# Kernel tuning notes

Hardware: AMD Instinct MI355X
Metric: run time of the kernel (lower is better)

## Reference

```python
import jax, jax.numpy as jnp
import numpy as np

B, TQ, TI, TT = 8, 256, 256, 256
H, NH, F, E = 1024, 16, 4096, 8
HD = H // NH
EPS = 1e-5


def _ln(x, g, b):
    m = x.mean(-1, keepdims=True)
    v = ((x - m) ** 2).mean(-1, keepdims=True)
    return (x - m) / jnp.sqrt(v + EPS) * g + b


def _mha(q, k, v, in_w, in_b, out_w, out_b):
    # torch nn.MultiheadAttention: packed in_proj [3H,H], out_proj [H,H]
    wq, wk, wv = jnp.split(in_w, 3, axis=0)
    bq, bk, bv = jnp.split(in_b, 3, axis=0)
    Bq, Tq, _ = q.shape
    Tk = k.shape[1]
    qh = (q @ wq.T + bq).reshape(Bq, Tq, NH, HD)
    kh = (k @ wk.T + bk).reshape(Bq, Tk, NH, HD)
    vh = (v @ wv.T + bv).reshape(Bq, Tk, NH, HD)
    scores = jnp.einsum('bqhd,bkhd->bhqk', qh, kh) / jnp.sqrt(jnp.float32(HD))
    attn = jax.nn.softmax(scores, axis=-1)
    out = jnp.einsum('bhqk,bkhd->bqhd', attn, vh).reshape(Bq, Tq, H)
    return out @ out_w.T + out_b


def _moe(x, w1, b1, w2, b2, probs):
    # dense all-expert FFN: GELU(x W1 + b1) W2 + b2, mixed by router probs
    h = jax.nn.gelu(jnp.einsum('bth,ehf->btef', x, w1) + b1, approximate=False)
    o = jnp.einsum('btef,efh->bteh', h, w2) + b2
    return (o * probs[..., None]).sum(axis=-2)


def setup_inputs() -> dict:
    key = jax.random.key(0)
    ks = jax.random.split(key, 24)
    s = 0.02
    d = {}
    d['query_tokens'] = jax.random.normal(ks[0], (B, TQ, H), jnp.float32)
    d['image_tokens'] = jax.random.normal(ks[1], (B, TI, H), jnp.float32)
    d['text_context'] = jax.random.normal(ks[2], (B, TT, H), jnp.float32)
    d['sa_in_w'] = jax.random.normal(ks[3], (3 * H, H), jnp.float32) * s
    d['sa_in_b'] = jnp.zeros((3 * H,), jnp.float32)
    d['sa_out_w'] = jax.random.normal(ks[4], (H, H), jnp.float32) * s
    d['sa_out_b'] = jnp.zeros((H,), jnp.float32)
    d['ca_in_w'] = jax.random.normal(ks[5], (3 * H, H), jnp.float32) * s
    d['ca_in_b'] = jnp.zeros((3 * H,), jnp.float32)
    d['ca_out_w'] = jax.random.normal(ks[6], (H, H), jnp.float32) * s
    d['ca_out_b'] = jnp.zeros((H,), jnp.float32)
    d['img_gate_w'] = jax.random.normal(ks[7], (E, 2 * H), jnp.float32) * s
    d['img_gate_b'] = jnp.zeros((E,), jnp.float32)
    d['txt_gate_w'] = jax.random.normal(ks[8], (E, 2 * H), jnp.float32) * s
    d['txt_gate_b'] = jnp.zeros((E,), jnp.float32)
    d['lnq_g'] = jnp.ones((H,), jnp.float32)
    d['lnq_b'] = jnp.zeros((H,), jnp.float32)
    d['lnc_g'] = jnp.ones((H,), jnp.float32)
    d['lnc_b'] = jnp.zeros((H,), jnp.float32)
    d['lnf_g'] = jnp.ones((H,), jnp.float32)
    d['lnf_b'] = jnp.zeros((H,), jnp.float32)
    d['ew1'] = jax.random.normal(ks[9], (E, H, F), jnp.float32) * s
    d['eb1'] = jnp.zeros((E, F), jnp.float32)
    d['ew2'] = jax.random.normal(ks[10], (E, F, H), jnp.float32) * s
    d['eb2'] = jnp.zeros((E, H), jnp.float32)
    return d


def reference(query_tokens, image_tokens, text_context,
              sa_in_w, sa_in_b, sa_out_w, sa_out_b,
              ca_in_w, ca_in_b, ca_out_w, ca_out_b,
              img_gate_w, img_gate_b, txt_gate_w, txt_gate_b,
              lnq_g, lnq_b, lnc_g, lnc_b, lnf_g, lnf_b,
              ew1, eb1, ew2, eb2):
    # self-attention on query stream (dropout is identity in eval)
    q_norm = _ln(query_tokens, lnq_g, lnq_b)
    query_tokens = query_tokens + _mha(q_norm, q_norm, q_norm, sa_in_w, sa_in_b, sa_out_w, sa_out_b)
    # cross-attention query -> image tokens
    cross_norm = _ln(query_tokens, lnc_g, lnc_b)
    query_tokens = query_tokens + _mha(cross_norm, image_tokens, image_tokens, ca_in_w, ca_in_b, ca_out_w, ca_out_b)
    # gating contexts
    image_ctx = image_tokens.mean(axis=1, keepdims=True)   # [B,1,H]
    text_ctx = text_context.mean(axis=1, keepdims=True)    # [B,1,H]
    img_gate_in = jnp.concatenate([image_tokens, jnp.broadcast_to(text_ctx, image_tokens.shape)], axis=-1)
    txt_gate_in = jnp.concatenate([query_tokens, jnp.broadcast_to(image_ctx, query_tokens.shape)], axis=-1)
    temp = jnp.maximum(jnp.float32(1.0), 0.001)  # router temperature buffer = 1.0
    image_probs = jax.nn.softmax((img_gate_in @ img_gate_w.T + img_gate_b) / temp, axis=-1)
    text_probs = jax.nn.softmax((txt_gate_in @ txt_gate_w.T + txt_gate_b) / temp, axis=-1)
    # dense MoE (ep_group is None -> all experts evaluated, mixed by full softmax)
    q_ffn = _ln(query_tokens, lnf_g, lnf_b)
    query_tokens = query_tokens + _moe(q_ffn, ew1, eb1, ew2, eb2, text_probs)
    image_tokens = image_tokens + _moe(image_tokens, ew1, eb1, ew2, eb2, image_probs)
    return query_tokens, image_tokens
```

## Files before the change

kernel.cpp:

```cpp
#include <hip/hip_runtime.h>
#include <math.h>

typedef unsigned short u16;
typedef __bf16 bf16x8 __attribute__((ext_vector_type(8)));
typedef float  f32x4  __attribute__((ext_vector_type(4)));
typedef unsigned short u16x8 __attribute__((ext_vector_type(8)));
typedef unsigned short u16x4 __attribute__((ext_vector_type(4)));

union B8 { u16x8 u; bf16x8 b; };

__device__ __forceinline__ u16 f2bf(float x) {
  unsigned int u = __float_as_uint(x);
  unsigned int r = (u + 0x7fffu + ((u >> 16) & 1u)) >> 16;
  return (u16)r;
}
__device__ __forceinline__ float bf2f(u16 h) {
  return __uint_as_float(((unsigned int)h) << 16);
}

__device__ __forceinline__ void gload16(const void* g, void* l) {
  __builtin_amdgcn_global_load_lds(
      (const __attribute__((address_space(1))) unsigned int*)g,
      (__attribute__((address_space(3))) unsigned int*)l, 16, 0, 0);
}

__device__ __forceinline__ void wait_tiles(int left) {
  if (left >= 2)      asm volatile("s_waitcnt vmcnt(8)" ::: "memory");
  else if (left == 1) asm volatile("s_waitcnt vmcnt(4)" ::: "memory");
  else                asm volatile("s_waitcnt vmcnt(0)" ::: "memory");
}

__global__ __launch_bounds__(256) void cast_kernel(const float* __restrict__ in,
                                                   u16* __restrict__ out, int n4) {
  int i = blockIdx.x * 256 + threadIdx.x;
  if (i >= n4) return;
  f32x4 v = *(const f32x4*)(in + (size_t)i * 4);
  u16x4 o;
  o[0] = f2bf(v[0]); o[1] = f2bf(v[1]); o[2] = f2bf(v[2]); o[3] = f2bf(v[3]);
  *(u16x4*)(out + (size_t)i * 4) = o;
}

__global__ void transpose_cast_kernel(const float* __restrict__ in, u16* __restrict__ out,
                                      int R, int C) {
  __shared__ float tile[32][33];
  int z = blockIdx.z;
  int r0 = blockIdx.y * 32, c0 = blockIdx.x * 32;
  const float* ip = in + (size_t)z * R * C;
  u16* op = out + (size_t)z * R * C;
  int tx = threadIdx.x, ty = threadIdx.y;
  #pragma unroll
  for (int i = 0; i < 32; i += 8)
    tile[ty + i][tx] = ip[(size_t)(r0 + ty + i) * C + c0 + tx];
  __syncthreads();
  #pragma unroll
  for (int i = 0; i < 32; i += 8)
    op[(size_t)(c0 + ty + i) * R + r0 + tx] = f2bf(tile[tx][ty + i]);
}

__global__ __launch_bounds__(256) void ln_kernel(const float* __restrict__ in,
                                                 const float* __restrict__ g,
                                                 const float* __restrict__ bt,
                                                 u16* __restrict__ out) {
  __shared__ float red[4];
  int row = blockIdx.x;
  int t = threadIdx.x;
  int lane = t & 63, wid = t >> 6;
  f32x4 x = *(const f32x4*)(in + (size_t)row * 1024 + t * 4);
  float s = x[0] + x[1] + x[2] + x[3];
  #pragma unroll
  for (int o = 32; o > 0; o >>= 1) s += __shfl_down(s, o, 64);
  if (lane == 0) red[wid] = s;
  __syncthreads();
  float mean = (red[0] + red[1] + red[2] + red[3]) * (1.0f / 1024.0f);
  __syncthreads();
  float d0 = x[0] - mean, d1 = x[1] - mean, d2 = x[2] - mean, d3 = x[3] - mean;
  float s2 = d0 * d0 + d1 * d1 + d2 * d2 + d3 * d3;
  #pragma unroll
  for (int o = 32; o > 0; o >>= 1) s2 += __shfl_down(s2, o, 64);
  if (lane == 0) red[wid] = s2;
  __syncthreads();
  float var = (red[0] + red[1] + red[2] + red[3]) * (1.0f / 1024.0f);
  float rstd = rsqrtf(var + 1e-5f);
  f32x4 gg = *(const f32x4*)(g + t * 4);
  f32x4 bb = *(const f32x4*)(bt + t * 4);
  u16x4 o;
  o[0] = f2bf(d0 * rstd * gg[0] + bb[0]);
  o[1] = f2bf(d1 * rstd * gg[1] + bb[1]);
  o[2] = f2bf(d2 * rstd * gg[2] + bb[2]);
  o[3] = f2bf(d3 * rstd * gg[3] + bb[3]);
  *(u16x4*)(out + (size_t)row * 1024 + t * 4) = o;
}

#define SRC_COL(t) ((((t) & 3) ^ (((t) >> 3) & 1) ^ ((((t) >> 4) & 1) << 1)) * 8)

template <int MODE>
__global__ __launch_bounds__(256, 2) void gemm_bt(const u16* __restrict__ A,
                                                  const u16* __restrict__ B,
                                                  const float* __restrict__ bias,
                                                  const float* __restrict__ extra,
                                                  void* __restrict__ out,
                                                  int M, int N, int K, int expert, int kChunk) {
  __shared__ u16 sm[32768];
  const int tid = threadIdx.x;
  const int lane = tid & 63;
  const int wid = tid >> 6;
  const int wr = wid >> 1, wc = wid & 1;
  const int l15 = lane & 15;
  const int kg = lane >> 4;
  const int kgr8 = (kg ^ ((lane >> 1) & 1) ^ (((lane >> 2) & 1) << 1)) * 8;

  const int nwg = gridDim.x * gridDim.y;
  const int bid = blockIdx.y * gridDim.x + blockIdx.x;
  const int swz = (bid & 7) * (nwg >> 3) + (bid >> 3);
  const int m0 = (swz / gridDim.x) * 128;
  const int n0 = (swz % gridDim.x) * 128;
  const int kOff = blockIdx.z * kChunk;

  f32x4 acc[4][4];
  #pragma unroll
  for (int i = 0; i < 4; i++)
    #pragma unroll
    for (int j = 0; j < 4; j++) acc[i][j] = f32x4{0.f, 0.f, 0.f, 0.f};

  const int sc = SRC_COL(tid);
  const u16* ga = A + (size_t)(m0 + (tid >> 2)) * K + sc + kOff;
  const u16* gb = B + (size_t)(n0 + (tid >> 2)) * K + sc + kOff;
  const size_t rowskip = (size_t)64 * K;

#define STG(b, kt)                                                  \
  do {                                                              \
    u16* d = sm + (b) * 8192 + wid * 512;                           \
    gload16(ga + (kt), d);                                          \
    gload16(ga + rowskip + (kt), d + 2048);                         \
    gload16(gb + (kt), d + 4096);                                   \
    gload16(gb + rowskip + (kt), d + 6144);                         \
  } while (0)

  const int NT = kChunk >> 5;
  STG(0, 0); STG(1, 32); STG(2, 64);
  for (int t = 0; t < NT; ++t) {
    wait_tiles(NT - 1 - t);
    __builtin_amdgcn_s_barrier();
    if (t + 3 < NT) STG((t + 3) & 3, (t + 3) * 32);
    __builtin_amdgcn_sched_barrier(0);
    __builtin_amdgcn_s_setprio(1);
    const u16* base = sm + (t & 3) * 8192;
    B8 af[4], bfr[4];
    #pragma unroll
    for (int i = 0; i < 4; i++) {
      af[i].u  = *(const u16x8*)(base + (wr * 64 + l15 + i * 16) * 32 + kgr8);
      bfr[i].u = *(const u16x8*)(base + 4096 + (wc * 64 + l15 + i * 16) * 32 + kgr8);
    }
    #pragma unroll
    for (int i = 0; i < 4; i++)
      #pragma unroll
      for (int j = 0; j < 4; j++)
        acc[i][j] = __builtin_amdgcn_mfma_f32_16x16x32_bf16(af[i].b, bfr[j].b, acc[i][j], 0, 0, 0);
    __builtin_amdgcn_s_setprio(0);
  }
#undef STG

  const bool z0 = (blockIdx.z == 0);
  const int orow0 = m0 + wr * 64 + (lane >> 4) * 4;
  const int ocol0 = n0 + wc * 64 + l15;

  if constexpr (MODE == 0) {
    __builtin_amdgcn_s_barrier();
    u16* rp = sm + wid * 1152;
    const int mrow0 = m0 + wr * 64;
    const int cbase = n0 + wc * 64;
    #pragma unroll
    for (int i = 0; i < 4; i++) {
      #pragma unroll
      for (int j = 0; j < 4; j++) {
        const float bb = bias[cbase + j * 16 + l15];
        #pragma unroll
        for (int p = 0; p < 4; p++)
          rp[((lane >> 4) * 4 + p) * 72 + j * 16 + l15] = f2bf(acc[i][j][p] + bb);
      }
      asm volatile("s_waitcnt lgkmcnt(0)" ::: "memory");
      #pragma unroll
      for (int rr = 0; rr < 4; rr++) {
        const int r16 = rr * 4 + (lane >> 4);
        u16x4 v4 = *(const u16x4*)&rp[r16 * 72 + l15 * 4];
        *(u16x4*)((u16*)out + (size_t)(mrow0 + i * 16 + r16) * N + cbase + l15 * 4) = v4;
      }
      asm volatile("s_waitcnt lgkmcnt(0)" ::: "memory");
    }
  } else {
    #pragma unroll
    for (int i = 0; i < 4; i++) {
      float pr_[4];
      if constexpr (MODE == 3) {
        #pragma unroll
        for (int p = 0; p < 4; p++)
          pr_[p] = extra[(size_t)(orow0 + i * 16 + p) * 8 + expert];
      }
      #pragma unroll
      for (int j = 0; j < 4; j++) {
        const int gcol = ocol0 + j * 16;
        const float bb = bias[gcol];
        #pragma unroll
        for (int p = 0; p < 4; p++) {
          const int grow = orow0 + i * 16 + p;
          const size_t off = (size_t)grow * N + gcol;
          float v = acc[i][j][p];
          if constexpr (MODE == 1) {
            atomicAdd(&((float*)out)[off], v + (z0 ? bb + extra[off] : 0.f));
          } else {
            atomicAdd(&((float*)out)[off], pr_[p] * (v + (z0 ? bb : 0.f)));
          }
        }
      }
    }
  }
}

__global__ __launch_bounds__(512, 2) void gemm256(const u16* __restrict__ A, int lda,
                                                  const u16* __restrict__ B, int ldb,
                                                  const float* __restrict__ bias,
                                                  void* __restrict__ out,
                                                  int N, int kChunk) {
  __shared__ u16 sm[65536];
  const int tid = threadIdx.x;
  const int lane = tid & 63;
  const int wid = tid >> 6;
  const int wr = wid >> 2;
  const int wc = wid & 3;
  const int l15 = lane & 15;
  const int kg = lane >> 4;
  const int kgr8 = (kg ^ ((lane >> 1) & 1) ^ (((lane >> 2) & 1) << 1)) * 8;

  const int nwg = gridDim.x * gridDim.y;
  const int bid = blockIdx.y * gridDim.x + blockIdx.x;
  const int swz = (bid & 7) * (nwg >> 3) + (bid >> 3);
  const int m0 = (swz / gridDim.x) * 256;
  const int n0 = (swz % gridDim.x) * 256;

  f32x4 acc[8][4];
  #pragma unroll
  for (int i = 0; i < 8; i++)
    #pragma unroll
    for (int j = 0; j < 4; j++) acc[i][j] = f32x4{0.f, 0.f, 0.f, 0.f};

  const int sc = SRC_COL(tid);
  const u16* ga = A + (size_t)(m0 + (tid >> 2)) * lda + sc;
  const u16* gb = B + (size_t)(n0 + (tid >> 2)) * ldb + sc;
  const size_t a128 = (size_t)128 * lda;
  const size_t b128 = (size_t)128 * ldb;

#define STG256(b, kt)                                               \
  do {                                                              \
    u16* d = sm + (b) * 16384 + wid * 512;                          \
    gload16(ga + (kt), d);                                          \
    gload16(ga + (kt) + a128, d + 4096);                            \
    gload16(gb + (kt), d + 8192);                                   \
    gload16(gb + (kt) + b128, d + 12288);                           \
  } while (0)

  const int NT = kChunk >> 5;
  STG256(0, 0); STG256(1, 32); STG256(2, 64);
  for (int t = 0; t < NT; ++t) {
    wait_tiles(NT - 1 - t);
    __builtin_amdgcn_s_barrier();
    if (t + 3 < NT) STG256((t + 3) & 3, (t + 3) * 32);
    __builtin_amdgcn_sched_barrier(0);
    __builtin_amdgcn_s_setprio(1);
    const u16* base = sm + (t & 3) * 16384;
    B8 af[8], bfr[4];
    #pragma unroll
    for (int j = 0; j < 4; j++)
      bfr[j].u = *(const u16x8*)(base + 8192 + (wc * 64 + l15 + j * 16) * 32 + kgr8);
    #pragma unroll
    for (int i = 0; i < 8; i++)
      af[i].u = *(const u16x8*)(base + (wr * 128 + l15 + i * 16) * 32 + kgr8);
    #pragma unroll
    for (int i = 0; i < 8; i++)
      #pragma unroll
      for (int j = 0; j < 4; j++)
        acc[i][j] = __builtin_amdgcn_mfma_f32_16x16x32_bf16(af[i].b, bfr[j].b, acc[i][j], 0, 0, 0);
    __builtin_amdgcn_s_setprio(0);
  }
#undef STG256

  __builtin_amdgcn_s_barrier();
  u16* rp = sm + wid * 1152;
  const int mrow0 = m0 + wr * 128;
  const int cbase = n0 + wc * 64;
  #pragma unroll
  for (int i = 0; i < 8; i++) {
    #pragma unroll
    for (int j = 0; j < 4; j++) {
      const float bb = bias[cbase + j * 16 + l15];
      #pragma unroll
      for (int p = 0; p < 4; p++) {
        float vb = acc[i][j][p] + bb;
        float ge = 0.5f * vb * (1.0f + erff(vb * 0.70710678118654752f));
        rp[((lane >> 4) * 4 + p) * 72 + j * 16 + l15] = f2bf(ge);
      }
    }
    asm volatile("s_waitcnt lgkmcnt(0)" ::: "memory");
    #pragma unroll
    for (int rr = 0; rr < 4; rr++) {
      const int r16 = rr * 4 + (lane >> 4);
      u16x4 v4 = *(const u16x4*)&rp[r16 * 72 + l15 * 4];
      *(u16x4*)((u16*)out + (size_t)(mrow0 + i * 16 + r16) * N + cbase + l15 * 4) = v4;
    }
    asm volatile("s_waitcnt lgkmcnt(0)" ::: "memory");
  }
}

__global__ __launch_bounds__(256) void attn_mfma(const u16* __restrict__ qb, int qs,
                                                 const u16* __restrict__ kb_, int ks,
                                                 const u16* __restrict__ vb, int vs,
                                                 u16* __restrict__ outp) {
  __shared__ u16 Ks[64][72];
  __shared__ u16 Vt[64][72];
  __shared__ u16 Pl[4][64][72];
  const int t = threadIdx.x;
  const int lane = t & 63;
  const int w = t >> 6;
  const int b = blockIdx.x >> 4;
  const int h = blockIdx.x & 15;
  const int lr = lane & 15;
  const int kg = lane >> 4;
  const size_t qrow0 = (size_t)b * 256 + w * 64;

  B8 qf[4][2];
  #pragma unroll
  for (int i = 0; i < 4; i++)
    #pragma unroll
    for (int kk = 0; kk < 2; kk++)
      qf[i][kk].u = *(const u16x8*)(qb + (qrow0 + i * 16 + lr) * qs + h * 64 + kk * 32 + kg * 8);

  f32x4 ao[4][4];
  float m_[4][4], l_[4][4];
  #pragma unroll
  for (int i = 0; i < 4; i++)
    #pragma unroll
    for (int n = 0; n < 4; n++) ao[i][n] = f32x4{0.f, 0.f, 0.f, 0.f};
  #pragma unroll
  for (int i = 0; i < 4; i++)
    #pragma unroll
    for (int p = 0; p < 4; p++) { m_[i][p] = -1e30f; l_[i][p] = 0.f; }

  for (int jt = 0; jt < 4; ++jt) {
    __syncthreads();
    {
      int r = t >> 2, c = (t & 3) * 16;
      const u16* src = kb_ + ((size_t)b * 256 + jt * 64 + r) * ks + h * 64 + c;
      *(u16x8*)&Ks[r][c] = *(const u16x8*)src;
      *(u16x8*)&Ks[r][c + 8] = *(const u16x8*)(src + 8);
      int jj = t & 63;
      const u16* vsrc = vb + ((size_t)b * 256 + jt * 64 + jj) * vs + h * 64 + w * 16;
      u16x8 v0 = *(const u16x8*)vsrc;
      u16x8 v1 = *(const u16x8*)(vsrc + 8);
      #pragma unroll
      for (int d = 0; d < 8; d++) Vt[w * 16 + d][jj] = v0[d];
      #pragma unroll
      for (int d = 0; d < 8; d++) Vt[w * 16 + 8 + d][jj] = v1[d];
    }
    __syncthreads();

    B8 kf[2][4];
    #pragma unroll
    for (int kk = 0; kk < 2; kk++)
      #pragma unroll
      for (int n = 0; n < 4; n++)
        kf[kk][n].u = *(const u16x8*)&Ks[n * 16 + lr][kk * 32 + kg * 8];

    #pragma unroll
    for (int i = 0; i < 4; i++) {
      f32x4 s[4];
      #pragma unroll
      for (int n = 0; n < 4; n++) s[n] = f32x4{0.f, 0.f, 0.f, 0.f};
      #pragma unroll
      for (int kk = 0; kk < 2; kk++)
        #pragma unroll
        for (int n = 0; n < 4; n++)
          s[n] = __builtin_amdgcn_mfma_f32_16x16x32_bf16(qf[i][kk].b, kf[kk][n].b, s[n], 0, 0, 0);
      #pragma unroll
      for (int p = 0; p < 4; p++) {
        float pm = fmaxf(fmaxf(s[0][p], s[1][p]), fmaxf(s[2][p], s[3][p])) * 0.125f;
        #pragma unroll
        for (int mk = 1; mk < 16; mk <<= 1) pm = fmaxf(pm, __shfl_xor(pm, mk, 16));
        float mn = fmaxf(m_[i][p], pm);
        float scl = __expf(m_[i][p] - mn);
        m_[i][p] = mn;
        float rs = 0.f;
        #pragma unroll
        for (int n = 0; n < 4; n++) {
          float e = __expf(s[n][p] * 0.125f - mn);
          Pl[w][i * 16 + kg * 4 + p][n * 16 + lr] = f2bf(e);
          rs += e;
        }
        #pragma unroll
        for (int mk = 1; mk < 16; mk <<= 1) rs += __shfl_xor(rs, mk, 16);
        l_[i][p] = l_[i][p] * scl + rs;
        #pragma unroll
        for (int n2 = 0; n2 < 4; n2++) ao[i][n2][p] *= scl;
      }
    }

    B8 vf[2][4];
    #pragma unroll
    for (int kk = 0; kk < 2; kk++)
      #pragma unroll
      for (int n2 = 0; n2 < 4; n2++)
        vf[kk][n2].u = *(const u16x8*)&Vt[n2 * 16 + lr][kk * 32 + kg * 8];
    #pragma unroll
    for (int i = 0; i < 4; i++) {
      #pragma unroll
      for (int kk = 0; kk < 2; kk++) {
        B8 pa;
        pa.u = *(const u16x8*)&Pl[w][i * 16 + lr][kk * 32 + kg * 8];
        #pragma unroll
        for (int n2 = 0; n2 < 4; n2++)
          ao[i][n2] = __builtin_amdgcn_mfma_f32_16x16x32_bf16(pa.b, vf[kk][n2].b, ao[i][n2], 0, 0, 0);
      }
    }
  }

  #pragma unroll
  for (int i = 0; i < 4; i++) {
    #pragma unroll
    for (int p = 0; p < 4; p++) {
      const float inv = 1.0f / l_[i][p];
      const size_t row = qrow0 + i * 16 + kg * 4 + p;
      #pragma unroll
      for (int n2 = 0; n2 < 4; n2++)
        outp[row * 1024 + h * 64 + n2 * 16 + lr] = f2bf(ao[i][n2][p] * inv);
    }
  }
}

__global__ __launch_bounds__(256) void mean2_kernel(const float* __restrict__ in,
                                                    float* __restrict__ out) {
  __shared__ float part[128];
  const int blk = blockIdx.x;
  const int b = blk >> 3, ch = blk & 7;
  const int t = threadIdx.x;
  const int col = ch * 128 + (t & 127);
  const int half = t >> 7;
  const float* p = in + (size_t)b * 262144 + (size_t)half * 131072 + col;
  float s = 0.f;
  for (int r = 0; r < 128; r++) s += p[(size_t)r * 1024];
  if (half) part[t & 127] = s;
  __syncthreads();
  if (!half) out[b * 1024 + col] = (s + part[t & 127]) * (1.0f / 256.0f);
}

__global__ __launch_bounds__(256) void gate_kernel(const float* __restrict__ x,
                                                   const float* __restrict__ ctx,
                                                   const float* __restrict__ gw,
                                                   const float* __restrict__ gb,
                                                   float* __restrict__ probs, int rowoff) {
  __shared__ float lg[8];
  const int tok = blockIdx.x;
  const int b = tok >> 8;
  const int t = threadIdx.x;
  const int e = t >> 5, sl = t & 31;
  const float* xr = x + (size_t)tok * 1024;
  const float* cr = ctx + (size_t)b * 1024;
  const float* wrow = gw + (size_t)e * 2048;
  float s = 0.f;
  for (int c = sl; c < 1024; c += 32) s += xr[c] * wrow[c] + cr[c] * wrow[1024 + c];
  #pragma unroll
  for (int o = 16; o > 0; o >>= 1) s += __shfl_down(s, o, 32);
  if (sl == 0) lg[e] = s + gb[e];
  __syncthreads();
  if (t == 0) {
    float mx = lg[0];
    #pragma unroll
    for (int i = 1; i < 8; i++) mx = fmaxf(mx, lg[i]);
    float ex[8], sum = 0.f;
    #pragma unroll
    for (int i = 0; i < 8; i++) { ex[i] = expf(lg[i] - mx); sum += ex[i]; }
    float inv = 1.0f / sum;
    #pragma unroll
    for (int i = 0; i < 8; i++) probs[(size_t)(rowoff + tok) * 8 + i] = ex[i] * inv;
  }
}

__global__ __launch_bounds__(256) void final_add_kernel(const float* __restrict__ q3,
                                                        const float* __restrict__ img,
                                                        const float* __restrict__ moe,
                                                        float* __restrict__ out) {
  size_t i = (size_t)blockIdx.x * 256 + threadIdx.x;
  f32x4 m4 = *(const f32x4*)(moe + i * 4);
  f32x4 a4 = (i < 524288) ? *(const f32x4*)(q3 + i * 4)
                          : *(const f32x4*)(img + (i - 524288) * 4);
  f32x4 r;
  r[0] = a4[0] + m4[0]; r[1] = a4[1] + m4[1]; r[2] = a4[2] + m4[2]; r[3] = a4[3] + m4[3];
  *(f32x4*)(out + i * 4) = r;
}

extern "C" void kernel_launch(void* const* d_in, const int* in_sizes, int n_in,
                              void* d_out, int out_size, void* d_ws, size_t ws_size,
                              hipStream_t stream) {
  const float* query_in = (const float*)d_in[0];
  const float* image_in = (const float*)d_in[1];
  const float* text_in  = (const float*)d_in[2];
  const float* sa_in_w  = (const float*)d_in[3];
  const float* sa_in_b  = (const float*)d_in[4];
  const float* sa_out_w = (const float*)d_in[5];
  const float* sa_out_b = (const float*)d_in[6];
  const float* ca_in_w  = (const float*)d_in[7];
  const float* ca_in_b  = (const float*)d_in[8];
  const float* ca_out_w = (const float*)d_in[9];
  const float* ca_out_b = (const float*)d_in[10];
  const float* img_gate_w = (const float*)d_in[11];
  const float* img_gate_b = (const float*)d_in[12];
  const float* txt_gate_w = (const float*)d_in[13];
  const float* txt_gate_b = (const float*)d_in[14];
  const float* lnq_g = (const float*)d_in[15];
  const float* lnq_b = (const float*)d_in[16];
  const float* lnc_g = (const float*)d_in[17];
  const float* lnc_b = (const float*)d_in[18];
  const float* lnf_g = (const float*)d_in[19];
  const float* lnf_b = (const float*)d_in[20];
  const float* ew1 = (const float*)d_in[21];
  const float* eb1 = (const float*)d_in[22];
  const float* ew2 = (const float*)d_in[23];
  const float* eb2 = (const float*)d_in[24];

  char* base = (char*)d_ws;
  size_t off = 0;
  auto alloc = [&](size_t bytes) -> char* {
    char* p = base + off;
    off += (bytes + 255) & ~(size_t)255;
    return p;
  };

  u16* wsa_in  = (u16*)alloc((size_t)3072 * 1024 * 2);
  u16* wsa_out = (u16*)alloc((size_t)1024 * 1024 * 2);
  u16* wca_in  = (u16*)alloc((size_t)3072 * 1024 * 2);
  u16* wca_out = (u16*)alloc((size_t)1024 * 1024 * 2);
  u16* w1T = (u16*)alloc((size_t)8 * 4096 * 1024 * 2);
  u16* w2T = (u16*)alloc((size_t)8 * 4096 * 1024 * 2);
  char* big = alloc((size_t)50331648);
  float* q3 = (float*)alloc((size_t)2048 * 1024 * 4);
  u16* xmoe = (u16*)alloc((size_t)4096 * 1024 * 2);
  float* probs = (float*)alloc((size_t)4096 * 8 * 4);
  float* ctx = (float*)alloc((size_t)2 * 8192 * 4);

  u16* h1      = (u16*)big;
  float* moeac = (float*)(big + 33554432);
  u16* qn      = (u16*)big;
  u16* qkv     = (u16*)(big + 4194304);
  u16* attn_o  = (u16*)(big + 16777216);
  float* q2    = (float*)(big + 20971520);
  u16* cnorm   = (u16*)(big + 29360128);
  u16* qca     = (u16*)(big + 33554432);
  u16* kvca    = (u16*)(big + 37748736);
  u16* img_bf  = xmoe + (size_t)2048 * 1024;

  cast_kernel<<<3072, 256, 0, stream>>>(sa_in_w, wsa_in, 786432);
  cast_kernel<<<1024, 256, 0, stream>>>(sa_out_w, wsa_out, 262144);
  cast_kernel<<<3072, 256, 0, stream>>>(ca_in_w, wca_in, 786432);
  cast_kernel<<<1024, 256, 0, stream>>>(ca_out_w, wca_out, 262144);
  transpose_cast_kernel<<<dim3(128, 32, 8), dim3(32, 8), 0, stream>>>(ew1, w1T, 1024, 4096);
  transpose_cast_kernel<<<dim3(32, 128, 8), dim3(32, 8), 0, stream>>>(ew2, w2T, 4096, 1024);
  cast_kernel<<<2048, 256, 0, stream>>>(image_in, img_bf, 524288);

  ln_kernel<<<2048, 256, 0, stream>>>(query_in, lnq_g, lnq_b, qn);
  gemm_bt<0><<<dim3(24, 16), 256, 0, stream>>>(qn, wsa_in, sa_in_b, nullptr, qkv, 2048, 3072, 1024, 0, 1024);
  attn_mfma<<<128, 256, 0, stream>>>(qkv, 3072, qkv + 1024, 3072, qkv + 2048, 3072, attn_o);
  hipMemsetAsync(q2, 0, (size_t)2048 * 1024 * 4, stream);
  gemm_bt<1><<<dim3(8, 16, 2), 256, 0, stream>>>(attn_o, wsa_out, sa_out_b, query_in, q2, 2048, 1024, 1024, 0, 512);

  ln_kernel<<<2048, 256, 0, stream>>>(q2, lnc_g, lnc_b, cnorm);
  gemm_bt<0><<<dim3(8, 16), 256, 0, stream>>>(cnorm, wca_in, ca_in_b, nullptr, qca, 2048, 1024, 1024, 0, 1024);
  gemm_bt<0><<<dim3(16, 16), 256, 0, stream>>>(img_bf, wca_in + (size_t)1024 * 1024,
                                               ca_in_b + 1024, nullptr, kvca, 2048, 2048, 1024, 0, 1024);
  attn_mfma<<<128, 256, 0, stream>>>(qca, 1024, kvca, 2048, kvca + 1024, 2048, attn_o);
  hipMemsetAsync(q3, 0, (size_t)2048 * 1024 * 4, stream);
  gemm_bt<1><<<dim3(8, 16, 2), 256, 0, stream>>>(attn_o, wca_out, ca_out_b, q2, q3, 2048, 1024, 1024, 0, 512);

  mean2_kernel<<<64, 256, 0, stream>>>(image_in, ctx);
  mean2_kernel<<<64, 256, 0, stream>>>(text_in, ctx + 8192);
  gate_kernel<<<2048, 256, 0, stream>>>(q3, ctx, txt_gate_w, txt_gate_b, probs, 0);
  gate_kernel<<<2048, 256, 0, stream>>>(image_in, ctx + 8192, img_gate_w, img_gate_b, probs, 2048);

  ln_kernel<<<2048, 256, 0, stream>>>(q3, lnf_g, lnf_b, xmoe);
  hipMemsetAsync(moeac, 0, (size_t)4096 * 1024 * 4, stream);
  for (int e = 0; e < 8; ++e) {
    gemm256<<<dim3(16, 16), 512, 0, stream>>>(xmoe, 1024, w1T + (size_t)e * 4194304, 1024,
                                              eb1 + (size_t)e * 4096, h1, 4096, 1024);
    gemm_bt<3><<<dim3(8, 32), 256, 0, stream>>>(h1, w2T + (size_t)e * 4194304,
                                                eb2 + (size_t)e * 1024, probs, moeac,
                                                4096, 1024, 4096, e, 4096);
  }

  final_add_kernel<<<4096, 256, 0, stream>>>(q3, image_in, moeac, (float*)d_out);
}
```

Measured before the change: 1.253 ms.

## Run MoE down-projection on split-K 256x256 GEMM with interleaved staged loads

The expert W2 GEMM moves from the 128x128 gemm_bt kernel to the 256x256 gemm256 kernel with 4-way split-K and atomic, probability-weighted accumulation. The gemm256 main loop is restructured: A and B tile prefetches are issued at separate points, the MFMA work is split into two halves with LDS fragment loads between them, and explicit vmcnt waits with barriers replace the wait_tiles helper. The LDS swizzle pattern is also simplified. This aims to raise MFMA utilisation and operand reuse for the large GEMMs, at the cost of more atomics and extra barriers per iteration.

```diff
diff --git a/kernel.cpp b/kernel.cpp
--- a/kernel.cpp
+++ b/kernel.cpp
@@ -91,7 +91,7 @@
   *(u16x4*)(out + (size_t)row * 1024 + t * 4) = o;
 }
 
-#define SRC_COL(t) ((((t) & 3) ^ (((t) >> 3) & 1) ^ ((((t) >> 4) & 1) << 1)) * 8)
+#define SRC_COL(t) ((((t) & 3) ^ (((t) >> 3) & 3)) * 8)
 
 template <int MODE>
 __global__ __launch_bounds__(256, 2) void gemm_bt(const u16* __restrict__ A,
@@ -107,7 +107,7 @@
   const int wr = wid >> 1, wc = wid & 1;
   const int l15 = lane & 15;
   const int kg = lane >> 4;
-  const int kgr8 = (kg ^ ((lane >> 1) & 1) ^ (((lane >> 2) & 1) << 1)) * 8;
+  const int kgr8 = (kg ^ ((lane >> 1) & 3)) * 8;
 
   const int nwg = gridDim.x * gridDim.y;
   const int bid = blockIdx.y * gridDim.x + blockIdx.x;
@@ -190,12 +190,6 @@
   } else {
     #pragma unroll
     for (int i = 0; i < 4; i++) {
-      float pr_[4];
-      if constexpr (MODE == 3) {
-        #pragma unroll
-        for (int p = 0; p < 4; p++)
-          pr_[p] = extra[(size_t)(orow0 + i * 16 + p) * 8 + expert];
-      }
       #pragma unroll
       for (int j = 0; j < 4; j++) {
         const int gcol = ocol0 + j * 16;
@@ -204,23 +198,20 @@
         for (int p = 0; p < 4; p++) {
           const int grow = orow0 + i * 16 + p;
           const size_t off = (size_t)grow * N + gcol;
-          float v = acc[i][j][p];
-          if constexpr (MODE == 1) {
-            atomicAdd(&((float*)out)[off], v + (z0 ? bb + extra[off] : 0.f));
-          } else {
-            atomicAdd(&((float*)out)[off], pr_[p] * (v + (z0 ? bb : 0.f)));
-          }
+          atomicAdd(&((float*)out)[off], acc[i][j][p] + (z0 ? bb + extra[off] : 0.f));
         }
       }
     }
   }
 }
 
+template <int MODE>
 __global__ __launch_bounds__(512, 2) void gemm256(const u16* __restrict__ A, int lda,
                                                   const u16* __restrict__ B, int ldb,
                                                   const float* __restrict__ bias,
+                                                  const float* __restrict__ extra,
                                                   void* __restrict__ out,
-                                                  int N, int kChunk) {
+                                                  int N, int kChunk, int expert) {
   __shared__ u16 sm[65536];
   const int tid = threadIdx.x;
   const int lane = tid & 63;
@@ -229,13 +220,14 @@
   const int wc = wid & 3;
   const int l15 = lane & 15;
   const int kg = lane >> 4;
-  const int kgr8 = (kg ^ ((lane >> 1) & 1) ^ (((lane >> 2) & 1) << 1)) * 8;
+  const int kgr8 = (kg ^ ((lane >> 1) & 3)) * 8;
 
   const int nwg = gridDim.x * gridDim.y;
   const int bid = blockIdx.y * gridDim.x + blockIdx.x;
   const int swz = (bid & 7) * (nwg >> 3) + (bid >> 3);
   const int m0 = (swz / gridDim.x) * 256;
   const int n0 = (swz % gridDim.x) * 256;
+  const int kOff = blockIdx.z * kChunk;
 
   f32x4 acc[8][4];
   #pragma unroll
@@ -244,69 +236,119 @@
     for (int j = 0; j < 4; j++) acc[i][j] = f32x4{0.f, 0.f, 0.f, 0.f};
 
   const int sc = SRC_COL(tid);
-  const u16* ga = A + (size_t)(m0 + (tid >> 2)) * lda + sc;
-  const u16* gb = B + (size_t)(n0 + (tid >> 2)) * ldb + sc;
+  const u16* ga = A + (size_t)(m0 + (tid >> 2)) * lda + sc + kOff;
+  const u16* gb = B + (size_t)(n0 + (tid >> 2)) * ldb + sc + kOff;
   const size_t a128 = (size_t)128 * lda;
   const size_t b128 = (size_t)128 * ldb;
 
-#define STG256(b, kt)                                               \
-  do {                                                              \
-    u16* d = sm + (b) * 16384 + wid * 512;                          \
-    gload16(ga + (kt), d);                                          \
-    gload16(ga + (kt) + a128, d + 4096);                            \
-    gload16(gb + (kt), d + 8192);                                   \
-    gload16(gb + (kt) + b128, d + 12288);                           \
-  } while (0)
-
   const int NT = kChunk >> 5;
-  STG256(0, 0); STG256(1, 32); STG256(2, 64);
+  #pragma unroll
+  for (int p = 0; p < 3; ++p) {
+    u16* dA = sm + p * 16384 + wid * 512;
+    u16* dB = dA + 8192;
+    const size_t kc = (size_t)p * 32;
+    gload16(ga + kc, dA); gload16(ga + kc + a128, dA + 4096);
+    gload16(gb + kc, dB); gload16(gb + kc + b128, dB + 4096);
+  }
+  asm volatile("s_waitcnt vmcnt(8)" ::: "memory");
+  __builtin_amdgcn_s_barrier();
+
   for (int t = 0; t < NT; ++t) {
-    wait_tiles(NT - 1 - t);
+    const u16* base = sm + (t & 3) * 16384;
+    const int pf = t + 3;
+    const size_t kc = (size_t)pf * 32;
+    if (pf < NT) {
+      u16* dA = sm + (pf & 3) * 16384 + wid * 512;
+      gload16(ga + kc, dA); gload16(ga + kc + a128, dA + 4096);
+    }
+    B8 bf[4], af[4];
+    #pragma unroll
+    for (int j = 0; j < 4; j++)
+      bf[j].u = *(const u16x8*)(base + 8192 + (wc * 64 + j * 16 + l15) * 32 + kgr8);
+    #pragma unroll
+    for (int i = 0; i < 4; i++)
+      af[i].u = *(const u16x8*)(base + (wr * 128 + i * 16 + l15) * 32 + kgr8);
     __builtin_amdgcn_s_barrier();
-    if (t + 3 < NT) STG256((t + 3) & 3, (t + 3) * 32);
+    asm volatile("s_waitcnt lgkmcnt(0)" ::: "memory");
     __builtin_amdgcn_sched_barrier(0);
     __builtin_amdgcn_s_setprio(1);
-    const u16* base = sm + (t & 3) * 16384;
-    B8 af[8], bfr[4];
-    #pragma unroll
-    for (int j = 0; j < 4; j++)
-      bfr[j].u = *(const u16x8*)(base + 8192 + (wc * 64 + l15 + j * 16) * 32 + kgr8);
-    #pragma unroll
-    for (int i = 0; i < 8; i++)
-      af[i].u = *(const u16x8*)(base + (wr * 128 + l15 + i * 16) * 32 + kgr8);
-    #pragma unroll
-    for (int i = 0; i < 8; i++)
+    #pragma unroll
+    for (int i = 0; i < 4; i++)
       #pragma unroll
       for (int j = 0; j < 4; j++)
-        acc[i][j] = __builtin_amdgcn_mfma_f32_16x16x32_bf16(af[i].b, bfr[j].b, acc[i][j], 0, 0, 0);
+        acc[i][j] = __builtin_amdgcn_mfma_f32_16x16x32_bf16(af[i].b, bf[j].b, acc[i][j], 0, 0, 0);
     __builtin_amdgcn_s_setprio(0);
-  }
-#undef STG256
-
-  __builtin_amdgcn_s_barrier();
-  u16* rp = sm + wid * 1152;
-  const int mrow0 = m0 + wr * 128;
-  const int cbase = n0 + wc * 64;
-  #pragma unroll
-  for (int i = 0; i < 8; i++) {
-    #pragma unroll
-    for (int j = 0; j < 4; j++) {
-      const float bb = bias[cbase + j * 16 + l15];
-      #pragma unroll
-      for (int p = 0; p < 4; p++) {
-        float vb = acc[i][j][p] + bb;
-        float ge = 0.5f * vb * (1.0f + erff(vb * 0.70710678118654752f));
-        rp[((lane >> 4) * 4 + p) * 72 + j * 16 + l15] = f2bf(ge);
-      }
-    }
+    if (pf < NT) {
+      u16* dB = sm + (pf & 3) * 16384 + 8192 + wid * 512;
+      gload16(gb + kc, dB); gload16(gb + kc + b128, dB + 4096);
+    }
+    B8 af2[4];
+    #pragma unroll
+    for (int i = 0; i < 4; i++)
+      af2[i].u = *(const u16x8*)(base + (wr * 128 + (i + 4) * 16 + l15) * 32 + kgr8);
+    __builtin_amdgcn_s_barrier();
     asm volatile("s_waitcnt lgkmcnt(0)" ::: "memory");
-    #pragma unroll
-    for (int rr = 0; rr < 4; rr++) {
-      const int r16 = rr * 4 + (lane >> 4);
-      u16x4 v4 = *(const u16x4*)&rp[r16 * 72 + l15 * 4];
-      *(u16x4*)((u16*)out + (size_t)(mrow0 + i * 16 + r16) * N + cbase + l15 * 4) = v4;
-    }
-    asm volatile("s_waitcnt lgkmcnt(0)" ::: "memory");
+    __builtin_amdgcn_sched_barrier(0);
+    __builtin_amdgcn_s_setprio(1);
+    #pragma unroll
+    for (int i = 0; i < 4; i++)
+      #pragma unroll
+      for (int j = 0; j < 4; j++)
+        acc[i + 4][j] = __builtin_amdgcn_mfma_f32_16x16x32_bf16(af2[i].b, bf[j].b, acc[i + 4][j], 0, 0, 0);
+    __builtin_amdgcn_s_setprio(0);
+    if (t + 3 < NT)      asm volatile("s_waitcnt vmcnt(8)" ::: "memory");
+    else if (t + 2 < NT) asm volatile("s_waitcnt vmcnt(4)" ::: "memory");
+    else                 asm volatile("s_waitcnt vmcnt(0)" ::: "memory");
+    __builtin_amdgcn_s_barrier();
+  }
+
+  const bool z0 = (blockIdx.z == 0);
+  if constexpr (MODE == 2) {
+    u16* rp = sm + wid * 1152;
+    const int mrow0 = m0 + wr * 128;
+    const int cbase = n0 + wc * 64;
+    #pragma unroll
+    for (int i = 0; i < 8; i++) {
+      #pragma unroll
+      for (int j = 0; j < 4; j++) {
+        const float bb = bias[cbase + j * 16 + l15];
+        #pragma unroll
+        for (int p = 0; p < 4; p++) {
+          float vb = acc[i][j][p] + bb;
+          float ge = 0.5f * vb * (1.0f + erff(vb * 0.70710678118654752f));
+          rp[((lane >> 4) * 4 + p) * 72 + j * 16 + l15] = f2bf(ge);
+        }
+      }
+      asm volatile("s_waitcnt lgkmcnt(0)" ::: "memory");
+      #pragma unroll
+      for (int rr = 0; rr < 4; rr++) {
+        const int r16 = rr * 4 + (lane >> 4);
+        u16x4 v4 = *(const u16x4*)&rp[r16 * 72 + l15 * 4];
+        *(u16x4*)((u16*)out + (size_t)(mrow0 + i * 16 + r16) * N + cbase + l15 * 4) = v4;
+      }
+      asm volatile("s_waitcnt lgkmcnt(0)" ::: "memory");
+    }
+  } else {
+    const int orow0 = m0 + wr * 128 + (lane >> 4) * 4;
+    const int ocol0 = n0 + wc * 64 + l15;
+    #pragma unroll
+    for (int i = 0; i < 8; i++) {
+      float pr_[4];
+      #pragma unroll
+      for (int p = 0; p < 4; p++)
+        pr_[p] = extra[(size_t)(orow0 + i * 16 + p) * 8 + expert];
+      #pragma unroll
+      for (int j = 0; j < 4; j++) {
+        const int gcol = ocol0 + j * 16;
+        const float bb = bias[gcol];
+        #pragma unroll
+        for (int p = 0; p < 4; p++) {
+          const int grow = orow0 + i * 16 + p;
+          const size_t off = (size_t)grow * N + gcol;
+          atomicAdd(&((float*)out)[off], pr_[p] * (acc[i][j][p] + (z0 ? bb : 0.f)));
+        }
+      }
+    }
   }
 }
 
@@ -585,11 +627,12 @@
   ln_kernel<<<2048, 256, 0, stream>>>(q3, lnf_g, lnf_b, xmoe);
   hipMemsetAsync(moeac, 0, (size_t)4096 * 1024 * 4, stream);
   for (int e = 0; e < 8; ++e) {
-    gemm256<<<dim3(16, 16), 512, 0, stream>>>(xmoe, 1024, w1T + (size_t)e * 4194304, 1024,
-                                              eb1 + (size_t)e * 4096, h1, 4096, 1024);
-    gemm_bt<3><<<dim3(8, 32), 256, 0, stream>>>(h1, w2T + (size_t)e * 4194304,
-                                                eb2 + (size_t)e * 1024, probs, moeac,
-                                                4096, 1024, 4096, e, 4096);
+    gemm256<2><<<dim3(16, 16), 512, 0, stream>>>(xmoe, 1024, w1T + (size_t)e * 4194304, 1024,
+                                                 eb1 + (size_t)e * 4096, nullptr, h1,
+                                                 4096, 1024, 0);
+    gemm256<3><<<dim3(4, 16, 4), 512, 0, stream>>>(h1, 4096, w2T + (size_t)e * 4194304, 4096,
+                                                   eb2 + (size_t)e * 1024, probs, moeac,
+                                                   1024, 1024, e);
   }
 
   final_add_kernel<<<4096, 256, 0, stream>>>(q3, image_in, moeac, (float*)d_out);
```

Result: slower. 1.422 ms (+13.5%).

## Batch MoE experts in pairs via z-dimension and drop the 256-tile GEMM

Applied to the files above, without the earlier changes.

Removes the dedicated 256x256 gemm256 kernel for the first expert GEMM and reuses the 128x128 gemm_bt template with a new GELU epilogue mode. A new ZB template flag lets blockIdx.z index experts with per-z strides, so each launch now covers two experts. This doubles the grid per launch and halves the number of launches, at the cost of a larger h1 scratch buffer and giving up the larger tile's operand reuse. It also changes the LDS swizzle pattern (SRC_COL/kgr8) to a two-bit XOR.

```diff
diff --git a/kernel.cpp b/kernel.cpp
--- a/kernel.cpp
+++ b/kernel.cpp
@@ -91,15 +91,17 @@
   *(u16x4*)(out + (size_t)row * 1024 + t * 4) = o;
 }
 
-#define SRC_COL(t) ((((t) & 3) ^ (((t) >> 3) & 1) ^ ((((t) >> 4) & 1) << 1)) * 8)
-
-template <int MODE>
+#define SRC_COL(t) ((((t) & 3) ^ (((t) >> 3) & 3)) * 8)
+
+template <int MODE, int ZB>
 __global__ __launch_bounds__(256, 2) void gemm_bt(const u16* __restrict__ A,
                                                   const u16* __restrict__ B,
                                                   const float* __restrict__ bias,
                                                   const float* __restrict__ extra,
                                                   void* __restrict__ out,
-                                                  int M, int N, int K, int expert, int kChunk) {
+                                                  int M, int N, int K, int expertBase,
+                                                  int kChunk, size_t saz, size_t sbz,
+                                                  int sbiasz, size_t soutz) {
   __shared__ u16 sm[32768];
   const int tid = threadIdx.x;
   const int lane = tid & 63;
@@ -107,14 +109,19 @@
   const int wr = wid >> 1, wc = wid & 1;
   const int l15 = lane & 15;
   const int kg = lane >> 4;
-  const int kgr8 = (kg ^ ((lane >> 1) & 1) ^ (((lane >> 2) & 1) << 1)) * 8;
+  const int kgr8 = (kg ^ ((lane >> 1) & 3)) * 8;
+  const int z = blockIdx.z;
+
+  if (ZB) { A += (size_t)z * saz; B += (size_t)z * sbz; bias += z * sbiasz; }
+  const int kOff = ZB ? 0 : z * kChunk;
+  const bool z0 = ZB ? true : (z == 0);
+  const int expert = expertBase + (ZB ? z : 0);
 
   const int nwg = gridDim.x * gridDim.y;
   const int bid = blockIdx.y * gridDim.x + blockIdx.x;
   const int swz = (bid & 7) * (nwg >> 3) + (bid >> 3);
   const int m0 = (swz / gridDim.x) * 128;
   const int n0 = (swz % gridDim.x) * 128;
-  const int kOff = blockIdx.z * kChunk;
 
   f32x4 acc[4][4];
   #pragma unroll
@@ -160,11 +167,11 @@
   }
 #undef STG
 
-  const bool z0 = (blockIdx.z == 0);
   const int orow0 = m0 + wr * 64 + (lane >> 4) * 4;
   const int ocol0 = n0 + wc * 64 + l15;
 
-  if constexpr (MODE == 0) {
+  if constexpr (MODE == 0 || MODE == 2) {
+    u16* outp = (u16*)out + (ZB ? (size_t)z * soutz : 0);
     __builtin_amdgcn_s_barrier();
     u16* rp = sm + wid * 1152;
     const int mrow0 = m0 + wr * 64;
@@ -175,19 +182,24 @@
       for (int j = 0; j < 4; j++) {
         const float bb = bias[cbase + j * 16 + l15];
         #pragma unroll
-        for (int p = 0; p < 4; p++)
-          rp[((lane >> 4) * 4 + p) * 72 + j * 16 + l15] = f2bf(acc[i][j][p] + bb);
+        for (int p = 0; p < 4; p++) {
+          float vb = acc[i][j][p] + bb;
+          if constexpr (MODE == 2)
+            vb = 0.5f * vb * (1.0f + erff(vb * 0.70710678118654752f));
+          rp[((lane >> 4) * 4 + p) * 72 + j * 16 + l15] = f2bf(vb);
+        }
       }
       asm volatile("s_waitcnt lgkmcnt(0)" ::: "memory");
       #pragma unroll
       for (int rr = 0; rr < 4; rr++) {
         const int r16 = rr * 4 + (lane >> 4);
         u16x4 v4 = *(const u16x4*)&rp[r16 * 72 + l15 * 4];
-        *(u16x4*)((u16*)out + (size_t)(mrow0 + i * 16 + r16) * N + cbase + l15 * 4) = v4;
+        *(u16x4*)(outp + (size_t)(mrow0 + i * 16 + r16) * N + cbase + l15 * 4) = v4;
       }
       asm volatile("s_waitcnt lgkmcnt(0)" ::: "memory");
     }
   } else {
+    float* outp = (float*)out + (ZB ? (size_t)z * soutz : 0);
     #pragma unroll
     for (int i = 0; i < 4; i++) {
       float pr_[4];
@@ -204,109 +216,14 @@
         for (int p = 0; p < 4; p++) {
           const int grow = orow0 + i * 16 + p;
           const size_t off = (size_t)grow * N + gcol;
-          float v = acc[i][j][p];
           if constexpr (MODE == 1) {
-            atomicAdd(&((float*)out)[off], v + (z0 ? bb + extra[off] : 0.f));
+            atomicAdd(&outp[off], acc[i][j][p] + (z0 ? bb + extra[off] : 0.f));
           } else {
-            atomicAdd(&((float*)out)[off], pr_[p] * (v + (z0 ? bb : 0.f)));
+            atomicAdd(&outp[off], pr_[p] * (acc[i][j][p] + bb));
           }
         }
       }
     }
-  }
-}
-
-__global__ __launch_bounds__(512, 2) void gemm256(const u16* __restrict__ A, int lda,
-                                                  const u16* __restrict__ B, int ldb,
-                                                  const float* __restrict__ bias,
-                                                  void* __restrict__ out,
-                                                  int N, int kChunk) {
-  __shared__ u16 sm[65536];
-  const int tid = threadIdx.x;
-  const int lane = tid & 63;
-  const int wid = tid >> 6;
-  const int wr = wid >> 2;
-  const int wc = wid & 3;
-  const int l15 = lane & 15;
-  const int kg = lane >> 4;
-  const int kgr8 = (kg ^ ((lane >> 1) & 1) ^ (((lane >> 2) & 1) << 1)) * 8;
-
-  const int nwg = gridDim.x * gridDim.y;
-  const int bid = blockIdx.y * gridDim.x + blockIdx.x;
-  const int swz = (bid & 7) * (nwg >> 3) + (bid >> 3);
-  const int m0 = (swz / gridDim.x) * 256;
-  const int n0 = (swz % gridDim.x) * 256;
-
-  f32x4 acc[8][4];
-  #pragma unroll
-  for (int i = 0; i < 8; i++)
-    #pragma unroll
-    for (int j = 0; j < 4; j++) acc[i][j] = f32x4{0.f, 0.f, 0.f, 0.f};
-
-  const int sc = SRC_COL(tid);
-  const u16* ga = A + (size_t)(m0 + (tid >> 2)) * lda + sc;
-  const u16* gb = B + (size_t)(n0 + (tid >> 2)) * ldb + sc;
-  const size_t a128 = (size_t)128 * lda;
-  const size_t b128 = (size_t)128 * ldb;
-
-#define STG256(b, kt)                                               \
-  do {                                                              \
-    u16* d = sm + (b) * 16384 + wid * 512;                          \
-    gload16(ga + (kt), d);                                          \
-    gload16(ga + (kt) + a128, d + 4096);                            \
-    gload16(gb + (kt), d + 8192);                                   \
-    gload16(gb + (kt) + b128, d + 12288);                           \
-  } while (0)
-
-  const int NT = kChunk >> 5;
-  STG256(0, 0); STG256(1, 32); STG256(2, 64);
-  for (int t = 0; t < NT; ++t) {
-    wait_tiles(NT - 1 - t);
-    __builtin_amdgcn_s_barrier();
-    if (t + 3 < NT) STG256((t + 3) & 3, (t + 3) * 32);
-    __builtin_amdgcn_sched_barrier(0);
-    __builtin_amdgcn_s_setprio(1);
-    const u16* base = sm + (t & 3) * 16384;
-    B8 af[8], bfr[4];
-    #pragma unroll
-    for (int j = 0; j < 4; j++)
-      bfr[j].u = *(const u16x8*)(base + 8192 + (wc * 64 + l15 + j * 16) * 32 + kgr8);
-    #pragma unroll
-    for (int i = 0; i < 8; i++)
-      af[i].u = *(const u16x8*)(base + (wr * 128 + l15 + i * 16) * 32 + kgr8);
-    #pragma unroll
-    for (int i = 0; i < 8; i++)
-      #pragma unroll
-      for (int j = 0; j < 4; j++)
-        acc[i][j] = __builtin_amdgcn_mfma_f32_16x16x32_bf16(af[i].b, bfr[j].b, acc[i][j], 0, 0, 0);
-    __builtin_amdgcn_s_setprio(0);
-  }
-#undef STG256
-
-  __builtin_amdgcn_s_barrier();
-  u16* rp = sm + wid * 1152;
-  const int mrow0 = m0 + wr * 128;
-  const int cbase = n0 + wc * 64;
-  #pragma unroll
-  for (int i = 0; i < 8; i++) {
-    #pragma unroll
-    for (int j = 0; j < 4; j++) {
-      const float bb = bias[cbase + j * 16 + l15];
-      #pragma unroll
-      for (int p = 0; p < 4; p++) {
-        float vb = acc[i][j][p] + bb;
-        float ge = 0.5f * vb * (1.0f + erff(vb * 0.70710678118654752f));
-        rp[((lane >> 4) * 4 + p) * 72 + j * 16 + l15] = f2bf(ge);
-      }
-    }
-    asm volatile("s_waitcnt lgkmcnt(0)" ::: "memory");
-    #pragma unroll
-    for (int rr = 0; rr < 4; rr++) {
-      const int r16 = rr * 4 + (lane >> 4);
-      u16x4 v4 = *(const u16x4*)&rp[r16 * 72 + l15 * 4];
-      *(u16x4*)((u16*)out + (size_t)(mrow0 + i * 16 + r16) * N + cbase + l15 * 4) = v4;
-    }
-    asm volatile("s_waitcnt lgkmcnt(0)" ::: "memory");
   }
 }
 
@@ -538,14 +455,13 @@
   u16* wca_out = (u16*)alloc((size_t)1024 * 1024 * 2);
   u16* w1T = (u16*)alloc((size_t)8 * 4096 * 1024 * 2);
   u16* w2T = (u16*)alloc((size_t)8 * 4096 * 1024 * 2);
-  char* big = alloc((size_t)50331648);
+  char* big = alloc((size_t)67108864);
   float* q3 = (float*)alloc((size_t)2048 * 1024 * 4);
   u16* xmoe = (u16*)alloc((size_t)4096 * 1024 * 2);
+  float* moeac = (float*)alloc((size_t)4096 * 1024 * 4);
   float* probs = (float*)alloc((size_t)4096 * 8 * 4);
   float* ctx = (float*)alloc((size_t)2 * 8192 * 4);
 
-  u16* h1      = (u16*)big;
-  float* moeac = (float*)(big + 33554432);
   u16* qn      = (u16*)big;
   u16* qkv     = (u16*)(big + 4194304);
   u16* attn_o  = (u16*)(big + 16777216);
@@ -553,6 +469,7 @@
   u16* cnorm   = (u16*)(big + 29360128);
   u16* qca     = (u16*)(big + 33554432);
   u16* kvca    = (u16*)(big + 37748736);
+  u16* h1p     = (u16*)big;
   u16* img_bf  = xmoe + (size_t)2048 * 1024;
 
   cast_kernel<<<3072, 256, 0, stream>>>(sa_in_w, wsa_in, 786432);
@@ -564,18 +481,23 @@
   cast_kernel<<<2048, 256, 0, stream>>>(image_in, img_bf, 524288);
 
   ln_kernel<<<2048, 256, 0, stream>>>(query_in, lnq_g, lnq_b, qn);
-  gemm_bt<0><<<dim3(24, 16), 256, 0, stream>>>(qn, wsa_in, sa_in_b, nullptr, qkv, 2048, 3072, 1024, 0, 1024);
+  gemm_bt<0, 0><<<dim3(24, 16), 256, 0, stream>>>(qn, wsa_in, sa_in_b, nullptr, qkv,
+                                                  2048, 3072, 1024, 0, 1024, 0, 0, 0, 0);
   attn_mfma<<<128, 256, 0, stream>>>(qkv, 3072, qkv + 1024, 3072, qkv + 2048, 3072, attn_o);
   hipMemsetAsync(q2, 0, (size_t)2048 * 1024 * 4, stream);
-  gemm_bt<1><<<dim3(8, 16, 2), 256, 0, stream>>>(attn_o, wsa_out, sa_out_b, query_in, q2, 2048, 1024, 1024, 0, 512);
+  gemm_bt<1, 0><<<dim3(8, 16, 2), 256, 0, stream>>>(attn_o, wsa_out, sa_out_b, query_in, q2,
+                                                    2048, 1024, 1024, 0, 512, 0, 0, 0, 0);
 
   ln_kernel<<<2048, 256, 0, stream>>>(q2, lnc_g, lnc_b, cnorm);
-  gemm_bt<0><<<dim3(8, 16), 256, 0, stream>>>(cnorm, wca_in, ca_in_b, nullptr, qca, 2048, 1024, 1024, 0, 1024);
-  gemm_bt<0><<<dim3(16, 16), 256, 0, stream>>>(img_bf, wca_in + (size_t)1024 * 1024,
-                                               ca_in_b + 1024, nullptr, kvca, 2048, 2048, 1024, 0, 1024);
+  gemm_bt<0, 0><<<dim3(8, 16), 256, 0, stream>>>(cnorm, wca_in, ca_in_b, nullptr, qca,
+                                                 2048, 1024, 1024, 0, 1024, 0, 0, 0, 0);
+  gemm_bt<0, 0><<<dim3(16, 16), 256, 0, stream>>>(img_bf, wca_in + (size_t)1024 * 1024,
+                                                  ca_in_b + 1024, nullptr, kvca,
+                                                  2048, 2048, 1024, 0, 1024, 0, 0, 0, 0);
   attn_mfma<<<128, 256, 0, stream>>>(qca, 1024, kvca, 2048, kvca + 1024, 2048, attn_o);
   hipMemsetAsync(q3, 0, (size_t)2048 * 1024 * 4, stream);
-  gemm_bt<1><<<dim3(8, 16, 2), 256, 0, stream>>>(attn_o, wca_out, ca_out_b, q2, q3, 2048, 1024, 1024, 0, 512);
+  gemm_bt<1, 0><<<dim3(8, 16, 2), 256, 0, stream>>>(attn_o, wca_out, ca_out_b, q2, q3,
+                                                    2048, 1024, 1024, 0, 512, 0, 0, 0, 0);
 
   mean2_kernel<<<64, 256, 0, stream>>>(image_in, ctx);
   mean2_kernel<<<64, 256, 0, stream>>>(text_in, ctx + 8192);
@@ -584,12 +506,15 @@
 
   ln_kernel<<<2048, 256, 0, stream>>>(q3, lnf_g, lnf_b, xmoe);
   hipMemsetAsync(moeac, 0, (size_t)4096 * 1024 * 4, stream);
-  for (int e = 0; e < 8; ++e) {
-    gemm256<<<dim3(16, 16), 512, 0, stream>>>(xmoe, 1024, w1T + (size_t)e * 4194304, 1024,
-                                              eb1 + (size_t)e * 4096, h1, 4096, 1024);
-    gemm_bt<3><<<dim3(8, 32), 256, 0, stream>>>(h1, w2T + (size_t)e * 4194304,
-                                                eb2 + (size_t)e * 1024, probs, moeac,
-                                                4096, 1024, 4096, e, 4096);
+  for (int e0 = 0; e0 < 8; e0 += 2) {
+    gemm_bt<2, 1><<<dim3(32, 32, 2), 256, 0, stream>>>(
+        xmoe, w1T + (size_t)e0 * 4194304, eb1 + (size_t)e0 * 4096, nullptr, h1p,
+        4096, 4096, 1024, e0, 1024,
+         0,  4194304,  4096,  16777216);
+    gemm_bt<3, 1><<<dim3(8, 32, 2), 256, 0, stream>>>(
+        h1p, w2T + (size_t)e0 * 4194304, eb2 + (size_t)e0 * 1024, probs, moeac,
+        4096, 1024, 4096, e0, 4096,
+         16777216,  4194304,  1024,  0);
   }
 
   final_add_kernel<<<4096, 256, 0, stream>>>(q3, image_in, moeac, (float*)d_out);
```

Measured after the change: 1.231 ms. About the same (-1.8%).
